# Optimization experiments

Measured on AMD Instinct MI355X. Metric: run time of the kernel, lower is better.

Reference implementation:

```python
import jax, jax.numpy as jnp
import numpy as np

B, S, D, R = 256, 512, 128, 2048
H = 0.5  # integration step


def setup_inputs() -> dict:
    key = jax.random.key(0)
    ks = jax.random.split(key, 14)
    u = lambda k, shape, lo, hi: jax.random.uniform(k, shape, jnp.float32, lo, hi)
    bd, br = 1.0 / np.sqrt(D), 1.0 / np.sqrt(R)
    return {
        "inputs": jax.random.normal(ks[0], (B, S, D), jnp.float32),
        # input oscillator params (size D)
        "omega_in": u(ks[1], (D,), 1.0, 3.0),
        "gamma_in": u(ks[2], (D,), 0.1, 0.5),
        "alpha_in": u(ks[3], (D,), 0.5, 1.5),
        # input projection Linear(D -> R), torch layout [out, in]
        "W_proj": u(ks[4], (R, D), -bd, bd),
        "b_proj": u(ks[5], (R,), -bd, bd),
        # fixed reservoir oscillator params (size R)
        "omega_res": u(ks[6], (R,), 1.0, 3.0),
        "gamma_res": u(ks[7], (R,), 0.1, 0.5),
        "alpha_res": u(ks[8], (R,), 0.5, 1.5),
        # output oscillator params (size R)
        "omega_out": u(ks[9], (R,), 1.0, 3.0),
        "gamma_out": u(ks[10], (R,), 0.1, 0.5),
        "alpha_out": u(ks[11], (R,), 0.5, 1.5),
        # readout Linear(R -> D)
        "W_read": u(ks[12], (D, R), -br, br),
        "b_read": u(ks[13], (D,), -br, br),
    }


def _osc_step(f, x, y, omega, gamma, alpha):
    # x' = x + h*y ; y' = y + h*(alpha*f - 2|gamma|*y - |omega|^2 * x), clamped to [-5,5]
    accel = alpha * f - 2.0 * jnp.abs(gamma) * y - jnp.abs(omega) ** 2 * x
    x_new = jnp.clip(x + H * y, -5.0, 5.0)
    y_new = jnp.clip(y + H * accel, -5.0, 5.0)
    return x_new, y_new


def reference(inputs, omega_in, gamma_in, alpha_in, W_proj, b_proj,
              omega_res, gamma_res, alpha_res, omega_out, gamma_out, alpha_out,
              W_read, b_read):
    inputs_t = jnp.transpose(inputs, (1, 0, 2))  # [S, B, D]

    def step(carry, inp_t):
        x_in, y_in, x_res, y_res, x_out, y_out = carry
        x_in, y_in = _osc_step(inp_t, x_in, y_in, omega_in, gamma_in, alpha_in)
        proj = x_in @ W_proj.T + b_proj                      # [B, R]
        x_res, y_res = _osc_step(proj, x_res, y_res, omega_res, gamma_res, alpha_res)
        x_out, y_out = _osc_step(x_res, x_out, y_out, omega_out, gamma_out, alpha_out)
        pred = x_out @ W_read.T + b_read                     # [B, D]
        mse_out = jnp.mean((x_out - x_res) ** 2)             # scalar per step
        return (x_in, y_in, x_res, y_res, x_out, y_out), (pred, x_in, mse_out)

    z_d = jnp.zeros((B, D), inputs.dtype)
    z_r = jnp.zeros((B, R), inputs.dtype)
    carry0 = (z_d, z_d, z_r, z_r, z_r, z_r)
    _, (preds_t, x_in_seq, mse_out_seq) = jax.lax.scan(step, carry0, inputs_t)

    preds = jnp.transpose(preds_t, (1, 0, 2))  # [B, S, D]
    # pc_loss_in = sum_{t<S-1} mean((x_in(t) - inputs(t+1))^2)
    pc_loss_in = jnp.sum(jnp.mean((x_in_seq[:-1] - inputs_t[1:]) ** 2, axis=(1, 2)))
    pc_loss_out = jnp.sum(mse_out_seq)
    return preds, pc_loss_in, pc_loss_out
```

## Files before the change

### kernel.cpp

```cpp
#include <hip/hip_runtime.h>
#include <hip/hip_bf16.h>

#define Bn 256
#define Sn 512
#define Dn 128
#define Rn 2048
#define TB 32
#define NBLK (Sn / TB)
#define LDX 136
#define LDP 2056
#define LDI 132
#define NT 1024

using bf16_t = __hip_bfloat16;
typedef short bf16x8 __attribute__((ext_vector_type(8)));
typedef float f32x4 __attribute__((ext_vector_type(4)));
typedef float f32x2 __attribute__((ext_vector_type(2)));

__device__ __forceinline__ f32x2 clip2(f32x2 v) {
  v = __builtin_elementwise_max(v, (f32x2)(-5.f));
  v = __builtin_elementwise_min(v, (f32x2)(5.f));
  return v;
}

__device__ __forceinline__ unsigned bf16rne(float f) {
  const unsigned u = __float_as_uint(f);
  return (u + 0x7fffu + ((u >> 16) & 1u)) >> 16;
}
__device__ __forceinline__ unsigned pack_bf16(f32x2 v) {
  return (bf16rne(v.y) << 16) | (bf16rne(v.x) & 0xffffu);
}

__global__ __launch_bounds__(256) void k_prep(const float* __restrict__ Wp,
                                              const float* __restrict__ Wr,
                                              bf16_t* __restrict__ Wp_b,
                                              bf16_t* __restrict__ Wr_b,
                                              float* __restrict__ losses) {
  const int i = blockIdx.x * 256 + threadIdx.x;
  Wp_b[i] = __float2bfloat16(Wp[i]);
  Wr_b[i] = __float2bfloat16(Wr[i]);
  if (i == 0) { losses[0] = 0.f; losses[1] = 0.f; }
}

__global__ __launch_bounds__(NT, 4) void k_fused(
    const float* __restrict__ inp,
    const float* __restrict__ om_i, const float* __restrict__ ga_i,
    const float* __restrict__ al_i,
    const bf16_t* __restrict__ Wp, const float* __restrict__ bp,
    const float* __restrict__ omr, const float* __restrict__ gar,
    const float* __restrict__ alr,
    const float* __restrict__ omo, const float* __restrict__ gao,
    const float* __restrict__ alo,
    const bf16_t* __restrict__ Wr, const float* __restrict__ br,
    float* __restrict__ preds, float* __restrict__ losses) {
  __shared__ bf16_t Xs[TB * LDX];
  __shared__ bf16_t PX[TB * LDP];
  __shared__ float bpS[Rn];
  __shared__ float brS[Dn];
  __shared__ float smi[16], smo[16];

  const int tid = threadIdx.x;
  const int b = blockIdx.x;
  const int wv = tid >> 6, lane = tid & 63;
  const int lr = lane & 15, lq = lane >> 4;

  for (int i = tid; i < Rn; i += NT) bpS[i] = bp[i];
  if (tid < Dn) brS[tid] = br[tid];

  float xi = 0.f, yi = 0.f, pc_in = 0.f;
  float w2i = 0.f, g2i = 0.f, ai = 0.f;
  if (tid < Dn) {
    w2i = om_i[tid] * om_i[tid];
    g2i = 2.f * fabsf(ga_i[tid]);
    ai = al_i[tid];
  }
  const float* inpb = inp + (size_t)b * Sn * Dn;

  const int r0 = tid * 2;
  f32x2 xr = (f32x2)0.f, yr = (f32x2)0.f, xo = (f32x2)0.f, yo = (f32x2)0.f;
  f32x2 w2r, g2r, arv, w2o, g2o, aov;
  {
    f32x2 t;
    t = *(const f32x2*)(omr + r0); w2r = t * t;
    t = *(const f32x2*)(gar + r0); g2r = __builtin_elementwise_abs(t) * 2.f;
    arv = *(const f32x2*)(alr + r0);
    t = *(const f32x2*)(omo + r0); w2o = t * t;
    t = *(const f32x2*)(gao + r0); g2o = __builtin_elementwise_abs(t) * 2.f;
    aov = *(const f32x2*)(alo + r0);
  }
  f32x2 pc_out2 = (f32x2)0.f;

  float* Is = (float*)PX;
  float* Pb = (float*)((char*)PX + 65536);

  __syncthreads();

  for (int blk = 0; blk < NBLK; ++blk) {
    const int t0 = blk * TB;

    {
      const float* src = inpb + (size_t)t0 * Dn;
      const int row = tid >> 5, c4 = (tid & 31) * 4;
      *(f32x4*)&Is[row * LDI + c4] = *(const f32x4*)(src + (size_t)row * Dn + c4);
    }
    __syncthreads();

    if (tid < Dn) {
#pragma unroll
      for (int tt = 0; tt < TB; ++tt) {
        const float f = Is[tt * LDI + tid];
        if (t0 + tt > 0) { const float e = xi - f; pc_in += e * e; }
        const float accel = ai * f - g2i * yi - w2i * xi;
        const float xn = fminf(fmaxf(xi + 0.5f * yi, -5.f), 5.f);
        const float yn = fminf(fmaxf(yi + 0.5f * accel, -5.f), 5.f);
        Xs[tt * LDX + tid] = __float2bfloat16(xn);
        xi = xn; yi = yn;
      }
    }
    __syncthreads();

    {
      bf16x8 af[2][4];
#pragma unroll
      for (int i = 0; i < 2; ++i)
#pragma unroll
        for (int k = 0; k < 4; ++k)
          af[i][k] = *(const bf16x8*)&Xs[(i * 16 + lr) * LDX + k * 32 + lq * 8];

      const int n0w = wv * 128;
      const bf16_t* wp_base = Wp + (size_t)(n0w + lr) * Dn + lq * 8;
      bf16x8 bf[2][4];
#pragma unroll
      for (int k = 0; k < 4; ++k) {
        bf[0][k] = *(const bf16x8*)(wp_base + (size_t)0 * 16 * Dn + k * 32);
        bf[1][k] = *(const bf16x8*)(wp_base + (size_t)1 * 16 * Dn + k * 32);
      }
      for (int j = 0; j < 8; ++j) {
        const int pb = j & 1;
        f32x4 acc[2] = {(f32x4)0.f, (f32x4)0.f};
#pragma unroll
        for (int k = 0; k < 4; ++k) {
          acc[0] = __builtin_amdgcn_mfma_f32_16x16x32_bf16(af[0][k], bf[pb][k], acc[0], 0, 0, 0);
          acc[1] = __builtin_amdgcn_mfma_f32_16x16x32_bf16(af[1][k], bf[pb][k], acc[1], 0, 0, 0);
        }
        if (j + 2 < 8) {
#pragma unroll
          for (int k = 0; k < 4; ++k)
            bf[pb][k] = *(const bf16x8*)(wp_base + (size_t)(j + 2) * 16 * Dn + k * 32);
        }
        const int col = n0w + j * 16 + lr;
        const float bv = bpS[col];
#pragma unroll
        for (int i = 0; i < 2; ++i)
#pragma unroll
          for (int r = 0; r < 4; ++r)
            PX[(i * 16 + lq * 4 + r) * LDP + col] = __float2bfloat16(acc[i][r] + bv);
      }
    }
    __syncthreads();

    {
      unsigned pk = *(unsigned*)&PX[0 * LDP + r0];
      for (int tt = 0; tt < TB; ++tt) {
        unsigned pk_n = pk;
        if (tt + 1 < TB) pk_n = *(unsigned*)&PX[(tt + 1) * LDP + r0];
        f32x2 pv;
        pv.x = __uint_as_float(pk << 16);
        pv.y = __uint_as_float(pk & 0xffff0000u);
        f32x2 acr = arv * pv - g2r * yr - w2r * xr;
        f32x2 xrn = clip2(xr + yr * 0.5f);
        f32x2 yrn = clip2(yr + acr * 0.5f);
        f32x2 aco = aov * xrn - g2o * yo - w2o * xo;
        f32x2 xon = clip2(xo + yo * 0.5f);
        f32x2 yon = clip2(yo + aco * 0.5f);
        f32x2 e = xon - xrn;
        pc_out2 += e * e;
        xr = xrn; yr = yrn; xo = xon; yo = yon;
        *(unsigned*)&PX[tt * LDP + r0] = pack_bf16(xon);
        pk = pk_n;
      }
    }
    __syncthreads();

    {
      const int ct = wv & 7, kh = wv >> 3;
      const int d0 = ct * 16;
      const int kbase = kh * 1024;
      const bf16_t* wr_base = Wr + (size_t)(d0 + lr) * Rn + kbase + lq * 8;
      f32x4 acc[2][2] = {{(f32x4)0.f, (f32x4)0.f}, {(f32x4)0.f, (f32x4)0.f}};
      bf16x8 bcur = *(const bf16x8*)(wr_base);
#pragma unroll 2
      for (int k0 = 0; k0 < 1024; k0 += 32) {
        bf16x8 bnxt = bcur;
        if (k0 + 32 < 1024) bnxt = *(const bf16x8*)(wr_base + k0 + 32);
        const int par = (k0 >> 5) & 1;
        bf16x8 a0 = *(const bf16x8*)&PX[(0 + lr) * LDP + kbase + k0 + lq * 8];
        bf16x8 a1 = *(const bf16x8*)&PX[(16 + lr) * LDP + kbase + k0 + lq * 8];
        acc[0][par] = __builtin_amdgcn_mfma_f32_16x16x32_bf16(a0, bcur, acc[0][par], 0, 0, 0);
        acc[1][par] = __builtin_amdgcn_mfma_f32_16x16x32_bf16(a1, bcur, acc[1][par], 0, 0, 0);
        bcur = bnxt;
      }
      f32x4 accs[2];
      accs[0] = acc[0][0] + acc[0][1];
      accs[1] = acc[1][0] + acc[1][1];
      if (kh == 1) {
#pragma unroll
        for (int i = 0; i < 2; ++i)
#pragma unroll
          for (int r = 0; r < 4; ++r)
            Pb[ct * 512 + (i * 16 + lq * 4 + r) * 16 + lr] = accs[i][r];
      }
      __syncthreads();
      if (kh == 0) {
        float* outb = preds + (size_t)b * Sn * Dn + (size_t)t0 * Dn;
        const int col = d0 + lr;
        const float bv = brS[col];
#pragma unroll
        for (int i = 0; i < 2; ++i)
#pragma unroll
          for (int r = 0; r < 4; ++r) {
            const int row = i * 16 + lq * 4 + r;
            outb[(size_t)row * Dn + col] = accs[i][r] + Pb[ct * 512 + row * 16 + lr] + bv;
          }
      }
    }
    __syncthreads();
  }

  float vi = pc_in;
  float vo = pc_out2.x + pc_out2.y;
#pragma unroll
  for (int o = 32; o > 0; o >>= 1) {
    vi += __shfl_down(vi, o, 64);
    vo += __shfl_down(vo, o, 64);
  }
  if (lane == 0) { smi[wv] = vi; smo[wv] = vo; }
  __syncthreads();
  if (tid == 0) {
    float si = 0.f, so = 0.f;
#pragma unroll
    for (int w = 0; w < 16; ++w) { si += smi[w]; so += smo[w]; }
    atomicAdd(losses + 0, si * (1.f / ((float)Bn * (float)Dn)));
    atomicAdd(losses + 1, so * (1.f / ((float)Bn * (float)Rn)));
  }
}

extern "C" void kernel_launch(void* const* d_in, const int* in_sizes, int n_in,
                              void* d_out, int out_size, void* d_ws, size_t ws_size,
                              hipStream_t stream) {
  const float* inputs    = (const float*)d_in[0];
  const float* omega_in  = (const float*)d_in[1];
  const float* gamma_in  = (const float*)d_in[2];
  const float* alpha_in  = (const float*)d_in[3];
  const float* W_proj    = (const float*)d_in[4];
  const float* b_proj    = (const float*)d_in[5];
  const float* omega_res = (const float*)d_in[6];
  const float* gamma_res = (const float*)d_in[7];
  const float* alpha_res = (const float*)d_in[8];
  const float* omega_out = (const float*)d_in[9];
  const float* gamma_out = (const float*)d_in[10];
  const float* alpha_out = (const float*)d_in[11];
  const float* W_read    = (const float*)d_in[12];
  const float* b_read    = (const float*)d_in[13];

  float* out = (float*)d_out;
  float* losses = out + (size_t)Bn * Sn * Dn;

  bf16_t* Wp_b = (bf16_t*)d_ws;
  bf16_t* Wr_b = Wp_b + (size_t)Rn * Dn;

  k_prep<<<1024, 256, 0, stream>>>(W_proj, W_read, Wp_b, Wr_b, losses);
  k_fused<<<Bn, NT, 0, stream>>>(inputs, omega_in, gamma_in, alpha_in,
                                 Wp_b, b_proj,
                                 omega_res, gamma_res, alpha_res,
                                 omega_out, gamma_out, alpha_out,
                                 Wr_b, b_read, out, losses);
}
```

Measured before the change: 804.6 us.

## Split reservoir dimension across two blocks per batch, combine readout via atomics

Each batch row is now handled by two 512-thread blocks, each owning half of the reservoir (1024 units), instead of one 1024-thread block. The readout partial sums are combined with global float atomicAdd into a preds buffer that a new kernel pre-fills with the readout bias. This gives more, smaller blocks and halves shared memory per block, which may raise occupancy. In exchange each block recomputes the input oscillator and reloads the inputs, and the change adds a full write pass over preds plus many global atomics.

Result: faster. 679.7 us (-15.5%).

```diff
diff --git a/kernel.cpp b/kernel.cpp
--- a/kernel.cpp
+++ b/kernel.cpp
@@ -8,9 +8,9 @@
 #define TB 32
 #define NBLK (Sn / TB)
 #define LDX 136
-#define LDP 2056
+#define LDPs 1028
 #define LDI 132
-#define NT 1024
+#define RG 1024
 
 using bf16_t = __hip_bfloat16;
 typedef short bf16x8 __attribute__((ext_vector_type(8)));
@@ -42,7 +42,14 @@
   if (i == 0) { losses[0] = 0.f; losses[1] = 0.f; }
 }
 
-__global__ __launch_bounds__(NT, 4) void k_fused(
+__global__ __launch_bounds__(256) void k_zero(float* __restrict__ preds,
+                                              const float* __restrict__ br) {
+  const int i = blockIdx.x * 256 + threadIdx.x;
+  const f32x4 bv = *(const f32x4*)(br + (i & 31) * 4);
+  *((f32x4*)preds + i) = bv;
+}
+
+__global__ __launch_bounds__(512, 4) void k_fused(
     const float* __restrict__ inp,
     const float* __restrict__ om_i, const float* __restrict__ ga_i,
     const float* __restrict__ al_i,
@@ -51,21 +58,20 @@
     const float* __restrict__ alr,
     const float* __restrict__ omo, const float* __restrict__ gao,
     const float* __restrict__ alo,
-    const bf16_t* __restrict__ Wr, const float* __restrict__ br,
+    const bf16_t* __restrict__ Wr,
     float* __restrict__ preds, float* __restrict__ losses) {
   __shared__ bf16_t Xs[TB * LDX];
-  __shared__ bf16_t PX[TB * LDP];
-  __shared__ float bpS[Rn];
-  __shared__ float brS[Dn];
-  __shared__ float smi[16], smo[16];
+  __shared__ bf16_t PX[TB * LDPs];
+  __shared__ float bpS[RG];
+  __shared__ float smi[8], smo[8];
 
   const int tid = threadIdx.x;
-  const int b = blockIdx.x;
+  const int b = blockIdx.x >> 1, g = blockIdx.x & 1;
+  const int rbase = g * RG;
   const int wv = tid >> 6, lane = tid & 63;
   const int lr = lane & 15, lq = lane >> 4;
 
-  for (int i = tid; i < Rn; i += NT) bpS[i] = bp[i];
-  if (tid < Dn) brS[tid] = br[tid];
+  for (int i = tid; i < RG; i += 512) bpS[i] = bp[rbase + i];
 
   float xi = 0.f, yi = 0.f, pc_in = 0.f;
   float w2i = 0.f, g2i = 0.f, ai = 0.f;
@@ -76,22 +82,21 @@
   }
   const float* inpb = inp + (size_t)b * Sn * Dn;
 
-  const int r0 = tid * 2;
+  const int rl = tid * 2;
   f32x2 xr = (f32x2)0.f, yr = (f32x2)0.f, xo = (f32x2)0.f, yo = (f32x2)0.f;
   f32x2 w2r, g2r, arv, w2o, g2o, aov;
   {
     f32x2 t;
-    t = *(const f32x2*)(omr + r0); w2r = t * t;
-    t = *(const f32x2*)(gar + r0); g2r = __builtin_elementwise_abs(t) * 2.f;
-    arv = *(const f32x2*)(alr + r0);
-    t = *(const f32x2*)(omo + r0); w2o = t * t;
-    t = *(const f32x2*)(gao + r0); g2o = __builtin_elementwise_abs(t) * 2.f;
-    aov = *(const f32x2*)(alo + r0);
+    t = *(const f32x2*)(omr + rbase + rl); w2r = t * t;
+    t = *(const f32x2*)(gar + rbase + rl); g2r = __builtin_elementwise_abs(t) * 2.f;
+    arv = *(const f32x2*)(alr + rbase + rl);
+    t = *(const f32x2*)(omo + rbase + rl); w2o = t * t;
+    t = *(const f32x2*)(gao + rbase + rl); g2o = __builtin_elementwise_abs(t) * 2.f;
+    aov = *(const f32x2*)(alo + rbase + rl);
   }
   f32x2 pc_out2 = (f32x2)0.f;
 
   float* Is = (float*)PX;
-  float* Pb = (float*)((char*)PX + 65536);
 
   __syncthreads();
 
@@ -100,8 +105,11 @@
 
     {
       const float* src = inpb + (size_t)t0 * Dn;
-      const int row = tid >> 5, c4 = (tid & 31) * 4;
-      *(f32x4*)&Is[row * LDI + c4] = *(const f32x4*)(src + (size_t)row * Dn + c4);
+      for (int i = tid; i < (TB * Dn) / 4; i += 512) {
+        const int row = i >> 5, c4 = (i & 31) * 4;
+        f32x4 v = __builtin_nontemporal_load((const f32x4*)(src + (size_t)row * Dn + c4));
+        *(f32x4*)&Is[row * LDI + c4] = v;
+      }
     }
     __syncthreads();
 
@@ -127,8 +135,8 @@
         for (int k = 0; k < 4; ++k)
           af[i][k] = *(const bf16x8*)&Xs[(i * 16 + lr) * LDX + k * 32 + lq * 8];
 
-      const int n0w = wv * 128;
-      const bf16_t* wp_base = Wp + (size_t)(n0w + lr) * Dn + lq * 8;
+      const int lb = wv * 128;
+      const bf16_t* wp_base = Wp + (size_t)(rbase + lb + lr) * Dn + lq * 8;
       bf16x8 bf[2][4];
 #pragma unroll
       for (int k = 0; k < 4; ++k) {
@@ -148,22 +156,22 @@
           for (int k = 0; k < 4; ++k)
             bf[pb][k] = *(const bf16x8*)(wp_base + (size_t)(j + 2) * 16 * Dn + k * 32);
         }
-        const int col = n0w + j * 16 + lr;
-        const float bv = bpS[col];
+        const int cl = lb + j * 16 + lr;
+        const float bv = bpS[cl];
 #pragma unroll
         for (int i = 0; i < 2; ++i)
 #pragma unroll
           for (int r = 0; r < 4; ++r)
-            PX[(i * 16 + lq * 4 + r) * LDP + col] = __float2bfloat16(acc[i][r] + bv);
-      }
-    }
-    __syncthreads();
-
-    {
-      unsigned pk = *(unsigned*)&PX[0 * LDP + r0];
+            PX[(i * 16 + lq * 4 + r) * LDPs + cl] = __float2bfloat16(acc[i][r] + bv);
+      }
+    }
+    __syncthreads();
+
+    {
+      unsigned pk = *(unsigned*)&PX[0 * LDPs + rl];
       for (int tt = 0; tt < TB; ++tt) {
         unsigned pk_n = pk;
-        if (tt + 1 < TB) pk_n = *(unsigned*)&PX[(tt + 1) * LDP + r0];
+        if (tt + 1 < TB) pk_n = *(unsigned*)&PX[(tt + 1) * LDPs + rl];
         f32x2 pv;
         pv.x = __uint_as_float(pk << 16);
         pv.y = __uint_as_float(pk & 0xffff0000u);
@@ -176,52 +184,38 @@
         f32x2 e = xon - xrn;
         pc_out2 += e * e;
         xr = xrn; yr = yrn; xo = xon; yo = yon;
-        *(unsigned*)&PX[tt * LDP + r0] = pack_bf16(xon);
+        *(unsigned*)&PX[tt * LDPs + rl] = pack_bf16(xon);
         pk = pk_n;
       }
     }
     __syncthreads();
 
     {
-      const int ct = wv & 7, kh = wv >> 3;
-      const int d0 = ct * 16;
-      const int kbase = kh * 1024;
-      const bf16_t* wr_base = Wr + (size_t)(d0 + lr) * Rn + kbase + lq * 8;
+      const int d0 = wv * 16;
+      const bf16_t* wr_base = Wr + (size_t)(d0 + lr) * Rn + rbase + lq * 8;
       f32x4 acc[2][2] = {{(f32x4)0.f, (f32x4)0.f}, {(f32x4)0.f, (f32x4)0.f}};
       bf16x8 bcur = *(const bf16x8*)(wr_base);
 #pragma unroll 2
-      for (int k0 = 0; k0 < 1024; k0 += 32) {
+      for (int k0 = 0; k0 < RG; k0 += 32) {
         bf16x8 bnxt = bcur;
-        if (k0 + 32 < 1024) bnxt = *(const bf16x8*)(wr_base + k0 + 32);
+        if (k0 + 32 < RG) bnxt = *(const bf16x8*)(wr_base + k0 + 32);
         const int par = (k0 >> 5) & 1;
-        bf16x8 a0 = *(const bf16x8*)&PX[(0 + lr) * LDP + kbase + k0 + lq * 8];
-        bf16x8 a1 = *(const bf16x8*)&PX[(16 + lr) * LDP + kbase + k0 + lq * 8];
+        bf16x8 a0 = *(const bf16x8*)&PX[(0 + lr) * LDPs + k0 + lq * 8];
+        bf16x8 a1 = *(const bf16x8*)&PX[(16 + lr) * LDPs + k0 + lq * 8];
         acc[0][par] = __builtin_amdgcn_mfma_f32_16x16x32_bf16(a0, bcur, acc[0][par], 0, 0, 0);
         acc[1][par] = __builtin_amdgcn_mfma_f32_16x16x32_bf16(a1, bcur, acc[1][par], 0, 0, 0);
         bcur = bnxt;
       }
-      f32x4 accs[2];
-      accs[0] = acc[0][0] + acc[0][1];
-      accs[1] = acc[1][0] + acc[1][1];
-      if (kh == 1) {
-#pragma unroll
-        for (int i = 0; i < 2; ++i)
-#pragma unroll
-          for (int r = 0; r < 4; ++r)
-            Pb[ct * 512 + (i * 16 + lq * 4 + r) * 16 + lr] = accs[i][r];
-      }
-      __syncthreads();
-      if (kh == 0) {
-        float* outb = preds + (size_t)b * Sn * Dn + (size_t)t0 * Dn;
-        const int col = d0 + lr;
-        const float bv = brS[col];
-#pragma unroll
-        for (int i = 0; i < 2; ++i)
-#pragma unroll
-          for (int r = 0; r < 4; ++r) {
-            const int row = i * 16 + lq * 4 + r;
-            outb[(size_t)row * Dn + col] = accs[i][r] + Pb[ct * 512 + row * 16 + lr] + bv;
-          }
+      float* outb = preds + (size_t)b * Sn * Dn + (size_t)t0 * Dn;
+      const int col = d0 + lr;
+#pragma unroll
+      for (int i = 0; i < 2; ++i) {
+        f32x4 a = acc[i][0] + acc[i][1];
+#pragma unroll
+        for (int r = 0; r < 4; ++r) {
+          const int row = i * 16 + lq * 4 + r;
+          atomicAdd(outb + (size_t)row * Dn + col, a[r]);
+        }
       }
     }
     __syncthreads();
@@ -239,8 +233,8 @@
   if (tid == 0) {
     float si = 0.f, so = 0.f;
 #pragma unroll
-    for (int w = 0; w < 16; ++w) { si += smi[w]; so += smo[w]; }
-    atomicAdd(losses + 0, si * (1.f / ((float)Bn * (float)Dn)));
+    for (int w = 0; w < 8; ++w) { si += smi[w]; so += smo[w]; }
+    if (g == 0) atomicAdd(losses + 0, si * (1.f / ((float)Bn * (float)Dn)));
     atomicAdd(losses + 1, so * (1.f / ((float)Bn * (float)Rn)));
   }
 }
@@ -270,9 +264,10 @@
   bf16_t* Wr_b = Wp_b + (size_t)Rn * Dn;
 
   k_prep<<<1024, 256, 0, stream>>>(W_proj, W_read, Wp_b, Wr_b, losses);
-  k_fused<<<Bn, NT, 0, stream>>>(inputs, omega_in, gamma_in, alpha_in,
-                                 Wp_b, b_proj,
-                                 omega_res, gamma_res, alpha_res,
-                                 omega_out, gamma_out, alpha_out,
-                                 Wr_b, b_read, out, losses);
-}
+  k_zero<<<(Bn * Sn * Dn / 4) / 256, 256, 0, stream>>>(out, b_read);
+  k_fused<<<Bn * 2, 512, 0, stream>>>(inputs, omega_in, gamma_in, alpha_in,
+                                      Wp_b, b_proj,
+                                      omega_res, gamma_res, alpha_res,
+                                      omega_out, gamma_out, alpha_out,
+                                      Wr_b, out, losses);
+}
```
